# Kernel optimization log

Hardware: AMD Instinct MI355X
Metric: run time of the kernel (lower is better)

The kernel has to match this reference:

```python
import jax, jax.numpy as jnp
import numpy as np

Q = 128


def _maxpool2(x):
    # 2x2 max pool, stride 2, NCHW
    return jax.lax.reduce_window(x, -jnp.inf, jax.lax.max,
                                 (1, 1, 2, 2), (1, 1, 2, 2), 'VALID')


def _conv(x, w, b):
    y = jax.lax.conv_general_dilated(x, w, window_strides=(1, 1), padding='VALID',
                                     dimension_numbers=('NCHW', 'OIHW', 'NCHW'))
    return y + b[None, :, None, None]


def setup_inputs() -> dict:
    key = jax.random.key(0)
    ks = jax.random.split(key, 16)
    B = 4096
    x = jax.random.normal(ks[0], (B, 1, 28, 28), dtype=jnp.float32)
    hash_idx1 = jax.random.randint(ks[1], (25,), 0, Q, dtype=jnp.int32)
    hash_idx2 = jax.random.randint(ks[2], (800,), 0, Q, dtype=jnp.int32)
    hash_idx3 = jax.random.randint(ks[3], (1024,), 0, Q, dtype=jnp.int32)
    # random +/-1 signs
    sgn1 = jnp.sign(jax.random.normal(ks[4], (25,), dtype=jnp.float32))
    sgn2 = jnp.sign(jax.random.normal(ks[5], (800,), dtype=jnp.float32))
    sgn3 = jnp.sign(jax.random.normal(ks[6], (1024,), dtype=jnp.float32))
    # compressed (sketched) parameters: one length-Q vector per output unit
    w1 = jax.random.normal(ks[7], (32, Q), dtype=jnp.float32) * 0.2
    b1 = jax.random.normal(ks[8], (32,), dtype=jnp.float32) * 0.05
    w2 = jax.random.normal(ks[9], (64, Q), dtype=jnp.float32) * 0.05
    b2 = jax.random.normal(ks[10], (64,), dtype=jnp.float32) * 0.05
    w3 = jax.random.normal(ks[11], (512, Q), dtype=jnp.float32) * 0.03
    b3 = jax.random.normal(ks[12], (512,), dtype=jnp.float32) * 0.05
    fc2_w = jax.random.normal(ks[13], (10, 512), dtype=jnp.float32) * 0.04
    fc2_b = jax.random.normal(ks[14], (10,), dtype=jnp.float32) * 0.05
    return {'x': x,
            'hash_idx1': hash_idx1, 'hash_idx2': hash_idx2, 'hash_idx3': hash_idx3,
            'sgn1': sgn1, 'sgn2': sgn2, 'sgn3': sgn3,
            'w1': w1, 'b1': b1, 'w2': w2, 'b2': b2, 'w3': w3, 'b3': b3,
            'fc2_w': fc2_w, 'fc2_b': fc2_b}


def reference(x, hash_idx1, hash_idx2, hash_idx3, sgn1, sgn2, sgn3,
              w1, b1, w2, b2, w3, b3, fc2_w, fc2_b):
    # SketchConv1: reconstruct dense weight via gather + sign flip
    wc1 = (w1[:, hash_idx1] * sgn1[None, :]).reshape(32, 1, 5, 5)
    h = jax.nn.relu(_maxpool2(_conv(x, wc1, b1)))          # (B,32,12,12)
    # SketchConv2
    wc2 = (w2[:, hash_idx2] * sgn2[None, :]).reshape(64, 32, 5, 5)
    h = jax.nn.relu(_maxpool2(_conv(h, wc2, b2)))          # (B,64,4,4)
    h = h.reshape(h.shape[0], -1)                          # (B,1024)
    # SketchLinear
    W3 = w3[:, hash_idx3] * sgn3[None, :]                  # (512,1024)
    h = jax.nn.relu(h @ W3.T + b3)                         # (B,512)
    logits = h @ fc2_w.T + fc2_b                           # (B,10)
    return jax.nn.log_softmax(logits, axis=1)
```

## Files before the change

kernel.cpp:

```cpp
#include <hip/hip_runtime.h>
#include <hip/hip_bf16.h>
#include <math.h>


typedef __attribute__((ext_vector_type(8))) short bf16x8;
typedef __attribute__((ext_vector_type(4))) float f32x4;

static __device__ inline ushort f2bfu(float v) {
    union { __hip_bfloat16 h; ushort u; } cv;
    cv.h = __float2bfloat16(v);
    return cv.u;
}


__global__ __launch_bounds__(256)
void k_reconstruct(const float* __restrict__ w1, const float* __restrict__ w2,
                   const float* __restrict__ w3,
                   const int* __restrict__ hi1, const int* __restrict__ hi2,
                   const int* __restrict__ hi3,
                   const float* __restrict__ s1, const float* __restrict__ s2,
                   const float* __restrict__ s3,
                   __hip_bfloat16* __restrict__ wc1f,
                   __hip_bfloat16* __restrict__ wc1s,
                   __hip_bfloat16* __restrict__ wc2f,
                   __hip_bfloat16* __restrict__ W3f) {
    const int t = blockIdx.x * blockDim.x + threadIdx.x;
    bf16x8 o;
    if (t < 256) {
        const bool shifted = t >= 128;
        const int u = t & 127;
        const int nt = u >> 6, lane = u & 63;
        const int quad = lane >> 4, l15 = lane & 15;
        const int oc = nt * 16 + l15;
        #pragma unroll
        for (int j = 0; j < 8; ++j) {
            int tt = quad * 8 + j;
            int ki = (tt * 43) >> 8;
            int kj = tt - 6 * ki;
            float v = 0.f;
            if (!shifted && ki < 5 && kj < 5) {
                int f = ki * 5 + kj;
                v = w1[oc * 128 + hi1[f]] * s1[f];
            } else if (shifted && ki < 5 && kj >= 1 && kj <= 5) {
                int f = ki * 5 + (kj - 1);
                v = w1[oc * 128 + hi1[f]] * s1[f];
            }
            o[j] = (short)f2bfu(v);
        }
        *(bf16x8*)((ushort*)(shifted ? wc1s : wc1f) + (size_t)u * 8) = o;
    } else if (t < 6656) {
        const int u = t - 256;
        const int l15 = u & 15, quad = (u >> 4) & 3;
        const int ntA = (u >> 6) & 3, tap = u >> 8;
        const int oc = ntA * 16 + l15;
        #pragma unroll
        for (int j = 0; j < 8; ++j) {
            int ic = quad * 8 + j;
            int f = ic * 25 + tap;
            o[j] = (short)f2bfu(w2[oc * 128 + hi2[f]] * s2[f]);
        }
        *(bf16x8*)((ushort*)wc2f + (size_t)u * 8) = o;
    } else if (t < 72192) {
        const int u = t - 6656;
        const int l15 = u & 15, quad = (u >> 4) & 3;
        const int kt = (u >> 6) & 31, ntile = u >> 11;
        const int n = ntile * 16 + l15;
        #pragma unroll
        for (int j = 0; j < 8; ++j) {
            int k = kt * 32 + quad * 8 + j;
            o[j] = (short)f2bfu(w3[n * 128 + hi3[k]] * s3[k]);
        }
        *(bf16x8*)((ushort*)W3f + (size_t)u * 8) = o;
    }
}

__global__ __launch_bounds__(512, 6)
void k_conv(const float* __restrict__ x,
            const __hip_bfloat16* __restrict__ wc1f,
            const __hip_bfloat16* __restrict__ wc1s,
            const __hip_bfloat16* __restrict__ wc2f,
            const float* __restrict__ b1, const float* __restrict__ b2,
            ushort* __restrict__ h2f) {
    __shared__ __align__(16) ushort s_xb[4 * 816];
    __shared__ __align__(16) ushort s_h1[16 * 1160];

    const int tid = threadIdx.x;
    const int b0 = blockIdx.x * 4;
    const int wave = tid >> 6, lane = tid & 63;
    const int l15 = lane & 15, quad = lane >> 4;

    {
        const float4* xg = (const float4*)(x + (size_t)b0 * 784);
        for (int i = tid; i < 784; i += 512) {
            float4 v = xg[i];
            int img = i / 196;
            int pos = (i - img * 196) * 4;
            ushort* dst = &s_xb[img * 816 + pos];
            dst[0] = f2bfu(v.x); dst[1] = f2bfu(v.y);
            dst[2] = f2bfu(v.z); dst[3] = f2bfu(v.w);
        }
        if (tid < 128) {
            int img = tid >> 5, k = tid & 31;
            s_xb[img * 816 + 784 + k] = 0;
        }
    }

    bf16x8 bw1[2], bw1s[2];
    float bb1[2];
    #pragma unroll
    for (int nt = 0; nt < 2; ++nt) {
        bw1[nt]  = *(const bf16x8*)((const ushort*)wc1f + (nt * 64 + lane) * 8);
        bw1s[nt] = *(const bf16x8*)((const ushort*)wc1s + (nt * 64 + lane) * 8);
        bb1[nt] = b1[nt * 16 + l15];
    }
    __syncthreads();

    {
        const int img = wave >> 1, half = wave & 1;
        const int sub = l15 & 3;
        const ushort* srcImg = s_xb + img * 816;
        int offr[4];
        #pragma unroll
        for (int r = 0; r < 4; ++r) {
            int t = quad * 8 + 2 * r;
            int row = (t * 43) >> 8;
            int col = t - 6 * row;
            offr[r] = row * 28 + col;
        }
        const int g0 = l15 >> 3, r0 = l15 & 7;
        #pragma unroll
        for (int ii = 0; ii < 18; ++ii) {
            const int i = half * 18 + ii;
            const int pb = 4 * i + (l15 >> 2);
            const int pi = (pb * 171) >> 11;
            const int pj = pb - 12 * pi;
            const int base_e = (2 * pi + (sub >> 1)) * 28 + 2 * pj;
            const ushort* p0 = srcImg + base_e;
            union { bf16x8 v; uint u[4]; } A;
            A.u[0] = *(const uint*)(p0 + offr[0]);
            A.u[1] = *(const uint*)(p0 + offr[1]);
            A.u[2] = *(const uint*)(p0 + offr[2]);
            A.u[3] = *(const uint*)(p0 + offr[3]);
            f32x4 z = {0.f, 0.f, 0.f, 0.f};
            f32x4 ce0 = __builtin_amdgcn_mfma_f32_16x16x32_bf16(A.v, bw1[0],  z, 0, 0, 0);
            f32x4 co0 = __builtin_amdgcn_mfma_f32_16x16x32_bf16(A.v, bw1s[0], z, 0, 0, 0);
            f32x4 ce1 = __builtin_amdgcn_mfma_f32_16x16x32_bf16(A.v, bw1[1],  z, 0, 0, 0);
            f32x4 co1 = __builtin_amdgcn_mfma_f32_16x16x32_bf16(A.v, bw1s[1], z, 0, 0, 0);
            const int pbo = 4 * i + quad;
            float m0 = fmaxf(fmaxf(ce0[0], co0[1]), fmaxf(ce0[2], co0[3]));
            float m1 = fmaxf(fmaxf(ce1[0], co1[1]), fmaxf(ce1[2], co1[3]));
            s_h1[(img * 4 + g0) * 1160 + pbo * 8 + r0]     = f2bfu(fmaxf(m0 + bb1[0], 0.f));
            s_h1[(img * 4 + 2 + g0) * 1160 + pbo * 8 + r0] = f2bfu(fmaxf(m1 + bb1[1], 0.f));
        }
    }
    __syncthreads();

    const int pr = wave >> 1, nh = wave & 1;
    const int sub2 = l15 & 3;
    const int ci2 = 2 * pr + (sub2 >> 1);
    const int cj2 = 2 * (l15 >> 2) + (sub2 & 1);
    const int posBase = (ci2 * 12 + cj2) * 8;

    f32x4 acc[4][2];
    float bb2[2];
    #pragma unroll
    for (int ntl = 0; ntl < 2; ++ntl) {
        bb2[ntl] = b2[(nh * 2 + ntl) * 16 + l15];
        #pragma unroll
        for (int img = 0; img < 4; ++img)
            acc[img][ntl] = (f32x4){0.f, 0.f, 0.f, 0.f};
    }

    #pragma unroll
    for (int tap = 0; tap < 25; ++tap) {
        const int ki = tap / 5, kj = tap % 5;
        const int off = (ki * 12 + kj) * 8;
        bf16x8 a[4];
        #pragma unroll
        for (int img = 0; img < 4; ++img)
            a[img] = *(const bf16x8*)&s_h1[(img * 4 + quad) * 1160 + posBase + off];
        #pragma unroll
        for (int ntl = 0; ntl < 2; ++ntl) {
            bf16x8 bf = *(const bf16x8*)((const ushort*)wc2f +
                          ((tap * 4 + nh * 2 + ntl) * 64 + lane) * 8);
            #pragma unroll
            for (int img = 0; img < 4; ++img)
                acc[img][ntl] = __builtin_amdgcn_mfma_f32_16x16x32_bf16(
                    a[img], bf, acc[img][ntl], 0, 0, 0);
        }
    }

    #pragma unroll
    for (int img = 0; img < 4; ++img) {
        const int img_g = b0 + img;
        const size_t base = (size_t)(img_g >> 4) * 16384 + (img_g & 15) * 8;
        #pragma unroll
        for (int ntl = 0; ntl < 2; ++ntl) {
            f32x4 c = acc[img][ntl];
            float m = fmaxf(fmaxf(c[0], c[1]), fmaxf(c[2], c[3]));
            float v = fmaxf(m + bb2[ntl], 0.f);
            const int k = (nh * 2 + ntl) * 256 + l15 * 16 + pr * 4 + quad;
            h2f[base + (size_t)(k >> 5) * 512 + ((k >> 3) & 3) * 128 + (k & 7)] =
                f2bfu(v);
        }
    }
}

__global__ __launch_bounds__(512, 4)
void k_fc(const ushort* __restrict__ h2f, const __hip_bfloat16* __restrict__ W3f,
          const float* __restrict__ b3, const float* __restrict__ fc2w,
          const float* __restrict__ fc2b, float* __restrict__ out) {
    __shared__ float s_h3[16 * 516];

    const int tid = threadIdx.x;
    const int wave = tid >> 6, lane = tid & 63;
    const int l15 = lane & 15, quad = lane >> 4;
    const int mBase = blockIdx.x * 16;

    f32x4 acc[4];
    #pragma unroll
    for (int ntl = 0; ntl < 4; ++ntl) acc[ntl] = (f32x4){0.f, 0.f, 0.f, 0.f};

    const ushort* aP = h2f + (size_t)blockIdx.x * 16384 + lane * 8;
    const ushort* bP[4];
    #pragma unroll
    for (int ntl = 0; ntl < 4; ++ntl)
        bP[ntl] = (const ushort*)W3f + ((size_t)(wave * 4 + ntl) * 2048 + lane) * 8;

    #pragma unroll 2
    for (int kt = 0; kt < 32; ++kt) {
        bf16x8 a = *(const bf16x8*)(aP + kt * 512);
        #pragma unroll
        for (int ntl = 0; ntl < 4; ++ntl) {
            bf16x8 bf = *(const bf16x8*)(bP[ntl] + kt * 512);
            acc[ntl] = __builtin_amdgcn_mfma_f32_16x16x32_bf16(a, bf, acc[ntl], 0, 0, 0);
        }
    }

    #pragma unroll
    for (int ntl = 0; ntl < 4; ++ntl) {
        int col = wave * 64 + ntl * 16 + l15;
        float bb = b3[col];
        #pragma unroll
        for (int r = 0; r < 4; ++r)
            s_h3[(quad * 4 + r) * 516 + col] = fmaxf(acc[ntl][r] + bb, 0.f);
    }
    __syncthreads();

    #pragma unroll
    for (int i2 = 0; i2 < 2; ++i2) {
        const int m = wave * 2 + i2;
        const float* hrow = &s_h3[m * 516];
        float4 h0 = *(const float4*)&hrow[lane * 8];
        float4 h1 = *(const float4*)&hrow[lane * 8 + 4];
        float lg[10];
        #pragma unroll
        for (int c = 0; c < 10; ++c) {
            float4 w0 = *(const float4*)&fc2w[c * 512 + lane * 8];
            float4 w1 = *(const float4*)&fc2w[c * 512 + lane * 8 + 4];
            float s = h0.x * w0.x + h0.y * w0.y + h0.z * w0.z + h0.w * w0.w
                    + h1.x * w1.x + h1.y * w1.y + h1.z * w1.z + h1.w * w1.w;
            s += __shfl_down(s, 32);
            s += __shfl_down(s, 16);
            s += __shfl_down(s, 8);
            s += __shfl_down(s, 4);
            s += __shfl_down(s, 2);
            s += __shfl_down(s, 1);
            lg[c] = s;
        }
        if (lane == 0) {
            float mx = -1e30f;
            #pragma unroll
            for (int c = 0; c < 10; ++c) { lg[c] += fc2b[c]; mx = fmaxf(mx, lg[c]); }
            float sum = 0.f;
            #pragma unroll
            for (int c = 0; c < 10; ++c) sum += expf(lg[c] - mx);
            float lse = mx + logf(sum);
            #pragma unroll
            for (int c = 0; c < 10; ++c)
                out[(size_t)(mBase + m) * 10 + c] = lg[c] - lse;
        }
    }
}

extern "C" void kernel_launch(void* const* d_in, const int* in_sizes, int n_in,
                              void* d_out, int out_size, void* d_ws, size_t ws_size,
                              hipStream_t stream) {
    const float* x    = (const float*)d_in[0];
    const int*   hi1  = (const int*)d_in[1];
    const int*   hi2  = (const int*)d_in[2];
    const int*   hi3  = (const int*)d_in[3];
    const float* s1   = (const float*)d_in[4];
    const float* s2   = (const float*)d_in[5];
    const float* s3   = (const float*)d_in[6];
    const float* w1   = (const float*)d_in[7];
    const float* b1   = (const float*)d_in[8];
    const float* w2   = (const float*)d_in[9];
    const float* b2   = (const float*)d_in[10];
    const float* w3   = (const float*)d_in[11];
    const float* b3   = (const float*)d_in[12];
    const float* fc2w = (const float*)d_in[13];
    const float* fc2b = (const float*)d_in[14];
    float* out = (float*)d_out;

    const int B = in_sizes[0] / 784;

    char* ws = (char*)d_ws;
    __hip_bfloat16* wc1f = (__hip_bfloat16*)(ws + 0);
    __hip_bfloat16* wc1s = (__hip_bfloat16*)(ws + 2048);
    __hip_bfloat16* wc2f = (__hip_bfloat16*)(ws + 4096);
    __hip_bfloat16* W3f  = (__hip_bfloat16*)(ws + 106496);
    ushort*         h2f  = (ushort*)(ws + 1155072);

    k_reconstruct<<<(72192 + 255) / 256, 256, 0, stream>>>(
        w1, w2, w3, hi1, hi2, hi3, s1, s2, s3, wc1f, wc1s, wc2f, W3f);
    k_conv<<<B / 4, 512, 0, stream>>>(x, wc1f, wc1s, wc2f, b1, b2, h2f);
    k_fc<<<B / 16, 512, 0, stream>>>(h2f, W3f, b3, fc2w, fc2b, out);
}
```

Baseline: 146.2 us.

## Split FC layer into split-K MFMA kernel plus separate fc2/log-softmax kernel

```diff
diff --git a/kernel.cpp b/kernel.cpp
--- a/kernel.cpp
+++ b/kernel.cpp
@@ -206,80 +206,95 @@
     }
 }
 
-__global__ __launch_bounds__(512, 4)
-void k_fc(const ushort* __restrict__ h2f, const __hip_bfloat16* __restrict__ W3f,
-          const float* __restrict__ b3, const float* __restrict__ fc2w,
-          const float* __restrict__ fc2b, float* __restrict__ out) {
-    __shared__ float s_h3[16 * 516];
-
+__global__ __launch_bounds__(1024)
+void k_fc1(const ushort* __restrict__ h2f, const __hip_bfloat16* __restrict__ W3f,
+           float* __restrict__ p, int pstride) {
     const int tid = threadIdx.x;
     const int wave = tid >> 6, lane = tid & 63;
     const int l15 = lane & 15, quad = lane >> 4;
     const int mBase = blockIdx.x * 16;
-
-    f32x4 acc[4];
-    #pragma unroll
-    for (int ntl = 0; ntl < 4; ++ntl) acc[ntl] = (f32x4){0.f, 0.f, 0.f, 0.f};
-
-    const ushort* aP = h2f + (size_t)blockIdx.x * 16384 + lane * 8;
-    const ushort* bP[4];
-    #pragma unroll
-    for (int ntl = 0; ntl < 4; ++ntl)
-        bP[ntl] = (const ushort*)W3f + ((size_t)(wave * 4 + ntl) * 2048 + lane) * 8;
-
-    #pragma unroll 2
-    for (int kt = 0; kt < 32; ++kt) {
-        bf16x8 a = *(const bf16x8*)(aP + kt * 512);
-        #pragma unroll
-        for (int ntl = 0; ntl < 4; ++ntl) {
-            bf16x8 bf = *(const bf16x8*)(bP[ntl] + kt * 512);
-            acc[ntl] = __builtin_amdgcn_mfma_f32_16x16x32_bf16(a, bf, acc[ntl], 0, 0, 0);
-        }
-    }
-
-    #pragma unroll
-    for (int ntl = 0; ntl < 4; ++ntl) {
-        int col = wave * 64 + ntl * 16 + l15;
-        float bb = b3[col];
+    const int k0 = blockIdx.y * 16;
+
+    f32x4 acc[2];
+    acc[0] = (f32x4){0.f, 0.f, 0.f, 0.f};
+    acc[1] = (f32x4){0.f, 0.f, 0.f, 0.f};
+
+    const ushort* aP  = h2f + (size_t)blockIdx.x * 16384 + (size_t)k0 * 512 + lane * 8;
+    const ushort* bP0 = (const ushort*)W3f + ((size_t)(wave * 2)     * 16384
+                                              + (size_t)k0 * 512 + lane * 8);
+    const ushort* bP1 = (const ushort*)W3f + ((size_t)(wave * 2 + 1) * 16384
+                                              + (size_t)k0 * 512 + lane * 8);
+    #pragma unroll 4
+    for (int kt = 0; kt < 16; ++kt) {
+        bf16x8 a   = *(const bf16x8*)(aP + kt * 512);
+        bf16x8 bf0 = *(const bf16x8*)(bP0 + kt * 512);
+        bf16x8 bf1 = *(const bf16x8*)(bP1 + kt * 512);
+        acc[0] = __builtin_amdgcn_mfma_f32_16x16x32_bf16(a, bf0, acc[0], 0, 0, 0);
+        acc[1] = __builtin_amdgcn_mfma_f32_16x16x32_bf16(a, bf1, acc[1], 0, 0, 0);
+    }
+
+    float* pOut = p + (size_t)blockIdx.y * pstride;
+    #pragma unroll
+    for (int ntl = 0; ntl < 2; ++ntl) {
+        const int col = wave * 32 + ntl * 16 + l15;
         #pragma unroll
         for (int r = 0; r < 4; ++r)
-            s_h3[(quad * 4 + r) * 516 + col] = fmaxf(acc[ntl][r] + bb, 0.f);
-    }
+            pOut[(size_t)(mBase + quad * 4 + r) * 512 + col] = acc[ntl][r];
+    }
+}
+
+__global__ __launch_bounds__(256)
+void k_fc2(const float* __restrict__ p, int pstride,
+           const float* __restrict__ b3, const float* __restrict__ fc2w,
+           const float* __restrict__ fc2b, float* __restrict__ out) {
+    __shared__ float s_w[5120];
+
+    const int tid = threadIdx.x;
+    for (int i = tid; i < 1280; i += 256)
+        ((float4*)s_w)[i] = ((const float4*)fc2w)[i];
     __syncthreads();
 
-    #pragma unroll
-    for (int i2 = 0; i2 < 2; ++i2) {
-        const int m = wave * 2 + i2;
-        const float* hrow = &s_h3[m * 516];
-        float4 h0 = *(const float4*)&hrow[lane * 8];
-        float4 h1 = *(const float4*)&hrow[lane * 8 + 4];
-        float lg[10];
+    const int m = tid >> 4, t16 = tid & 15;
+    const int img = blockIdx.x * 16 + m;
+
+    float acc[10];
+    #pragma unroll
+    for (int c = 0; c < 10; ++c) acc[c] = 0.f;
+    #pragma unroll
+    for (int kb = 0; kb < 8; ++kb) {
+        const int k = kb * 64 + t16 * 4;
+        float4 v0 = *(const float4*)&p[(size_t)img * 512 + k];
+        float4 v1 = *(const float4*)&p[(size_t)pstride + (size_t)img * 512 + k];
+        float4 bb = *(const float4*)&b3[k];
+        float4 h;
+        h.x = fmaxf(v0.x + v1.x + bb.x, 0.f);
+        h.y = fmaxf(v0.y + v1.y + bb.y, 0.f);
+        h.z = fmaxf(v0.z + v1.z + bb.z, 0.f);
+        h.w = fmaxf(v0.w + v1.w + bb.w, 0.f);
         #pragma unroll
         for (int c = 0; c < 10; ++c) {
-            float4 w0 = *(const float4*)&fc2w[c * 512 + lane * 8];
-            float4 w1 = *(const float4*)&fc2w[c * 512 + lane * 8 + 4];
-            float s = h0.x * w0.x + h0.y * w0.y + h0.z * w0.z + h0.w * w0.w
-                    + h1.x * w1.x + h1.y * w1.y + h1.z * w1.z + h1.w * w1.w;
-            s += __shfl_down(s, 32);
-            s += __shfl_down(s, 16);
-            s += __shfl_down(s, 8);
-            s += __shfl_down(s, 4);
-            s += __shfl_down(s, 2);
-            s += __shfl_down(s, 1);
-            lg[c] = s;
-        }
-        if (lane == 0) {
-            float mx = -1e30f;
-            #pragma unroll
-            for (int c = 0; c < 10; ++c) { lg[c] += fc2b[c]; mx = fmaxf(mx, lg[c]); }
-            float sum = 0.f;
-            #pragma unroll
-            for (int c = 0; c < 10; ++c) sum += expf(lg[c] - mx);
-            float lse = mx + logf(sum);
-            #pragma unroll
-            for (int c = 0; c < 10; ++c)
-                out[(size_t)(mBase + m) * 10 + c] = lg[c] - lse;
-        }
+            float4 w = *(const float4*)&s_w[c * 512 + k];
+            acc[c] += h.x * w.x + h.y * w.y + h.z * w.z + h.w * w.w;
+        }
+    }
+    #pragma unroll
+    for (int c = 0; c < 10; ++c) {
+        acc[c] += __shfl_down(acc[c], 8, 16);
+        acc[c] += __shfl_down(acc[c], 4, 16);
+        acc[c] += __shfl_down(acc[c], 2, 16);
+        acc[c] += __shfl_down(acc[c], 1, 16);
+    }
+    if (t16 == 0) {
+        float l[10], mx = -1e30f;
+        #pragma unroll
+        for (int c = 0; c < 10; ++c) { l[c] = acc[c] + fc2b[c]; mx = fmaxf(mx, l[c]); }
+        float sum = 0.f;
+        #pragma unroll
+        for (int c = 0; c < 10; ++c) sum += expf(l[c] - mx);
+        float lse = mx + logf(sum);
+        #pragma unroll
+        for (int c = 0; c < 10; ++c)
+            out[(size_t)img * 10 + c] = l[c] - lse;
     }
 }
 
@@ -311,9 +326,11 @@
     __hip_bfloat16* wc2f = (__hip_bfloat16*)(ws + 4096);
     __hip_bfloat16* W3f  = (__hip_bfloat16*)(ws + 106496);
     ushort*         h2f  = (ushort*)(ws + 1155072);
+    float*          p    = (float*)(ws + 1155072 + (size_t)B * 2048);
 
     k_reconstruct<<<(72192 + 255) / 256, 256, 0, stream>>>(
         w1, w2, w3, hi1, hi2, hi3, s1, s2, s3, wc1f, wc1s, wc2f, W3f);
     k_conv<<<B / 4, 512, 0, stream>>>(x, wc1f, wc1s, wc2f, b1, b2, h2f);
-    k_fc<<<B / 16, 512, 0, stream>>>(h2f, W3f, b3, fc2w, fc2b, out);
-}
+    k_fc1<<<dim3(B / 16, 2), 1024, 0, stream>>>(h2f, W3f, p, B * 512);
+    k_fc2<<<B / 16, 256, 0, stream>>>(p, B * 512, b3, fc2w, fc2b, out);
+}
```

New measurement: 151.8 us. 3.8% more time.
